# Optimization experiments

Measured on AMD Instinct MI355X. Metric: run time of the kernel, lower is better.

## Reference

```python
import jax, jax.numpy as jnp
import numpy as np

B, S, D = 4, 256, 768      # batch, seq, activation_dim
F = 8192                   # dict_size (both modules)
K = 64                     # topk
C = 128                    # connections per downstream feature


def _topk_keep(post, k):
    """Keep top-k entries per row, zero elsewhere. post: [N, F]."""
    vals, idx = jax.lax.top_k(post, k)
    n = post.shape[0]
    return jnp.zeros_like(post).at[jnp.arange(n)[:, None], idx].set(vals)


def setup_inputs() -> dict:
    key = jax.random.key(0)
    ks = jax.random.split(key, 10)
    s = 1.0 / np.sqrt(D)
    return {
        "initial_acts": jax.random.normal(ks[0], (B, S, D), jnp.float32),
        "x_up": jax.random.normal(ks[1], (B, S, D), jnp.float32),
        "ln_scale": jax.random.uniform(ks[2], (B, S), jnp.float32, 0.5, 1.5),
        "W_enc_up": jax.random.normal(ks[3], (F, D), jnp.float32) * s,
        "b_enc_up": jnp.zeros((F,), jnp.float32),
        "W_dec_up": jax.random.normal(ks[4], (D, F), jnp.float32) * s,
        "b_dec_up": jax.random.normal(ks[5], (D,), jnp.float32) * 0.01,
        "W_enc_down": jax.random.normal(ks[6], (F, D), jnp.float32) * s,
        "b_enc_down": jnp.zeros((F,), jnp.float32),
        "W_dec_down": jax.random.normal(ks[7], (D, F), jnp.float32) * s,
        "b_dec_down": jax.random.normal(ks[8], (D,), jnp.float32) * 0.01,
        "conn": jax.random.randint(ks[9], (F, C), 0, F),  # all valid (no -1 pad)
    }


def reference(initial_acts, x_up, ln_scale,
              W_enc_up, b_enc_up, W_dec_up, b_dec_up,
              W_enc_down, b_enc_down, W_dec_down, b_dec_down,
              conn):
    b, s, d = initial_acts.shape
    n = b * s
    x0 = initial_acts.reshape(n, d)
    xu = x_up.reshape(n, d)
    ln = ln_scale.reshape(n)

    # --- vanilla_forward on upstream: TopK SAE encode + decode ---
    post_up = jax.nn.relu((xu - b_dec_up) @ W_enc_up.T + b_enc_up)  # [n, F]
    feat_up = _topk_keep(post_up, K)
    recon_up = feat_up @ W_dec_up.T + b_dec_up                      # [n, d]

    # --- pruned downstream path ---
    fd = W_enc_down.shape[0]
    fu = W_dec_up.shape[1]
    # virtual weights: down_encoder @ up_decoder  -> [F_down, F_up]
    virtual = W_enc_down @ W_dec_up
    # connection mask from index tensor [F_down, C]
    mask = jnp.zeros((fd, fu), bool).at[jnp.arange(fd)[:, None], conn].set(True)
    masked = jnp.where(mask, virtual, jnp.zeros((), virtual.dtype))

    approx = x0 @ W_enc_down.T                                      # initial contributions [n, F_down]
    approx = approx + feat_up @ masked.T + W_enc_down @ b_dec_up    # pruned contributions + b_dec term
    approx = approx / ln[:, None] + b_enc_down - W_enc_down @ b_dec_down

    feat_down = _topk_keep(approx, K)
    recon_down = feat_down @ W_dec_down.T + b_dec_down              # [n, d]

    return jnp.stack([recon_up.reshape(b, s, d), recon_down.reshape(b, s, d)])
```

## Files before the change

kernel.cpp:

```cpp
#include <hip/hip_runtime.h>


#define NTOK 1024
#define DIM  768
#define FF   8192
#define KK   64
#define CC   128
#define KSEL_UP 80
#define KSEL_DN 80
#define CAP  128

typedef unsigned short u16;
typedef unsigned int   u32;
typedef __attribute__((ext_vector_type(8))) short short8;
typedef __attribute__((ext_vector_type(4))) float floatx4;

__device__ __forceinline__ float bits2f(u32 v) {
    float f; __builtin_memcpy(&f, &v, 4); return f;
}
__device__ __forceinline__ u32 f2bits(float f) {
    u32 u; __builtin_memcpy(&u, &f, 4); return u;
}
__device__ __forceinline__ float bf2f(u16 u) { return bits2f(((u32)u) << 16); }
__device__ __forceinline__ u16 f2bf(float f) {
    u32 u = f2bits(f);
    u32 lsb = (u >> 16) & 1u;
    u += 0x7fffu + lsb;
    return (u16)(u >> 16);
}
__device__ __forceinline__ u16 f2h(float f) {
    _Float16 h = (_Float16)f;
    u16 u; __builtin_memcpy(&u, &h, 2); return u;
}
__device__ __forceinline__ float h2f(u16 u) {
    _Float16 h; __builtin_memcpy(&h, &u, 2); return (float)h;
}
__device__ __forceinline__ u16 hkey(u16 b) {
    return (b & 0x8000u) ? (u16)~b : (u16)(b | 0x8000u);
}
__device__ __forceinline__ u16 hunkey(u16 k) {
    return (k & 0x8000u) ? (u16)(k ^ 0x8000u) : (u16)~k;
}
__device__ __forceinline__ double dot4d(float4 x, float4 w) {
    return (double)x.x * w.x + (double)x.y * w.y
         + (double)x.z * w.z + (double)x.w * w.w;
}

__global__ __launch_bounds__(256) void convert_kernel(const float* __restrict__ src,
                                                      u16* __restrict__ dst, int n4) {
    int i = blockIdx.x * 256 + threadIdx.x;
    if (i < n4) {
        float4 v = ((const float4*)src)[i];
        ushort4 o;
        o.x = f2bf(v.x); o.y = f2bf(v.y); o.z = f2bf(v.z); o.w = f2bf(v.w);
        ((ushort4*)dst)[i] = o;
    }
}

__global__ __launch_bounds__(256) void transpose_kernel(const float* __restrict__ in,
                                                        float* __restrict__ out) {
    __shared__ float tile[32][33];
    int f0 = blockIdx.x * 32, d0 = blockIdx.y * 32;
    int tx = threadIdx.x, ty = threadIdx.y;
#pragma unroll
    for (int i = 0; i < 4; ++i)
        tile[ty + 8 * i][tx] = in[(size_t)(d0 + ty + 8 * i) * FF + f0 + tx];
    __syncthreads();
#pragma unroll
    for (int i = 0; i < 4; ++i)
        out[(size_t)(f0 + ty + 8 * i) * DIM + d0 + tx] = tile[tx][ty + 8 * i];
}

__global__ __launch_bounds__(256) void transpose16_kernel(const float* __restrict__ in,
                                                          u16* __restrict__ out) {
    __shared__ float tile[32][33];
    int f0 = blockIdx.x * 32, d0 = blockIdx.y * 32;
    int tx = threadIdx.x, ty = threadIdx.y;
#pragma unroll
    for (int i = 0; i < 4; ++i)
        tile[ty + 8 * i][tx] = in[(size_t)(d0 + ty + 8 * i) * FF + f0 + tx];
    __syncthreads();
#pragma unroll
    for (int i = 0; i < 4; ++i)
        out[(size_t)(f0 + ty + 8 * i) * DIM + d0 + tx] = f2bf(tile[tx][ty + 8 * i]);
}

__global__ __launch_bounds__(64) void bias_kernel(const float* __restrict__ Weu,
                                                  const float* __restrict__ Wed,
                                                  const float* __restrict__ bdu,
                                                  const float* __restrict__ bdd,
                                                  const float* __restrict__ bed,
                                                  float* __restrict__ sF,
                                                  float* __restrict__ tuF,
                                                  float* __restrict__ c2F,
                                                  double* __restrict__ s64,
                                                  double* __restrict__ tu64,
                                                  double* __restrict__ td64) {
    int f = blockIdx.x, lane = threadIdx.x;
    double su = 0.0, tu = 0.0, td = 0.0;
    for (int i = lane; i < DIM; i += 64) {
        double bu = (double)bdu[i], bd = (double)bdd[i];
        su += (double)Weu[(size_t)f * DIM + i] * bu;
        double w = (double)Wed[(size_t)f * DIM + i];
        tu += w * bu;
        td += w * bd;
    }
#pragma unroll
    for (int off = 32; off; off >>= 1) {
        su += __shfl_xor(su, off);
        tu += __shfl_xor(tu, off);
        td += __shfl_xor(td, off);
    }
    if (lane == 0) {
        sF[f] = (float)su; tuF[f] = (float)tu;
        c2F[f] = (float)((double)bed[f] - td);
        s64[f] = su; tu64[f] = tu; td64[f] = td;
    }
}

template <int MODE>
__global__ __launch_bounds__(256) void gemm16(const u16* __restrict__ A16,
                                              const u16* __restrict__ Bg16,
                                              u16* __restrict__ Sout,
                                              const float* __restrict__ sF,
                                              const float* __restrict__ b_enc) {
    __shared__ __align__(16) u16 As[128 * 40];
    __shared__ __align__(16) u16 Bs[128 * 40];
    int tid = threadIdx.x;
    int wave = tid >> 6, lane = tid & 63;
    int lm = lane & 15, quad = lane >> 4;
    int m0 = blockIdx.y * 128, n0 = blockIdx.x * 128;
    int wm = (wave >> 1) * 64, wn = (wave & 1) * 64;
    floatx4 acc[4][4];
#pragma unroll
    for (int i = 0; i < 4; ++i)
#pragma unroll
        for (int j = 0; j < 4; ++j)
            acc[i][j] = (floatx4){0.f, 0.f, 0.f, 0.f};
    int r = tid >> 2;
    int s = (tid & 3) * 8;
    const u16* gA = A16 + (size_t)(m0 + r) * DIM + s;
    const u16* gB = Bg16 + (size_t)(n0 + r) * DIM + s;
    for (int k0 = 0; k0 < DIM; k0 += 32) {
        short8 a0 = *(const short8*)(gA + k0);
        short8 a1 = *(const short8*)(gA + (size_t)64 * DIM + k0);
        short8 b0 = *(const short8*)(gB + k0);
        short8 b1 = *(const short8*)(gB + (size_t)64 * DIM + k0);
        __syncthreads();
        *(short8*)&As[r * 40 + s]        = a0;
        *(short8*)&As[(r + 64) * 40 + s] = a1;
        *(short8*)&Bs[r * 40 + s]        = b0;
        *(short8*)&Bs[(r + 64) * 40 + s] = b1;
        __syncthreads();
        short8 af[4], bfr[4];
#pragma unroll
        for (int mi = 0; mi < 4; ++mi)
            af[mi] = *(const short8*)&As[(wm + mi * 16 + lm) * 40 + quad * 8];
#pragma unroll
        for (int ni = 0; ni < 4; ++ni)
            bfr[ni] = *(const short8*)&Bs[(wn + ni * 16 + lm) * 40 + quad * 8];
#pragma unroll
        for (int mi = 0; mi < 4; ++mi)
#pragma unroll
            for (int ni = 0; ni < 4; ++ni)
                acc[mi][ni] = __builtin_amdgcn_mfma_f32_16x16x32_bf16(
                    af[mi], bfr[ni], acc[mi][ni], 0, 0, 0);
    }
#pragma unroll
    for (int ni = 0; ni < 4; ++ni) {
        int col = n0 + wn + ni * 16 + lm;
        float sub = 0.f, bb = 0.f;
        if (MODE == 0) { sub = sF[col]; bb = b_enc[col]; }
#pragma unroll
        for (int mi = 0; mi < 4; ++mi) {
#pragma unroll
            for (int reg = 0; reg < 4; ++reg) {
                int row = m0 + wm + mi * 16 + quad * 4 + reg;
                float v = acc[mi][ni][reg];
                if (MODE == 0) { v = v - sub + bb; v = v > 0.f ? v : 0.f; }
                Sout[(size_t)row * FF + col] = f2h(v);
            }
        }
    }
}

__device__ void find_threshold(u32* hist, int k, u32* sc) {
    int tid = threadIdx.x;
    for (int st = 1; st < 256; st <<= 1) {
        u32 v = 0;
        if (tid < 256) {
            v = hist[tid];
            if (tid + st < 256) v += hist[tid + st];
        }
        __syncthreads();
        if (tid < 256) hist[tid] = v;
        __syncthreads();
    }
    if (tid < 256) {
        u32 ge = hist[tid];
        u32 gn = (tid < 255) ? hist[tid + 1] : 0u;
        if ((int)ge >= k && (int)gn < k) { sc[0] = (u32)tid; sc[1] = (u32)(k - (int)gn); }
    }
    __syncthreads();
}

template <typename KT>
__device__ void radix_collect(const KT* __restrict__ keys, u32* hist, int* eqidx,
                              u32* sc, int ksel, u16* cr, u16* cv,
                              int* cnt_out, int row) {
    int tid = threadIdx.x, bs = blockDim.x;
    if (tid < 256) hist[tid] = 0;
    __syncthreads();
    for (int i = tid; i < FF; i += bs) atomicAdd(&hist[((u32)keys[i] & 0xffffu) >> 8], 1u);
    __syncthreads();
    find_threshold(hist, ksel, sc);
    int hb = (int)sc[0], k1 = (int)sc[1];
    if (tid < 256) hist[tid] = 0;
    __syncthreads();
    for (int i = tid; i < FF; i += bs) {
        u32 k = (u32)keys[i] & 0xffffu;
        if ((int)(k >> 8) == hb) atomicAdd(&hist[k & 255u], 1u);
    }
    __syncthreads();
    find_threshold(hist, k1, sc);
    u32 T = ((u32)hb << 8) | sc[0];
    if (tid == 0) { sc[2] = 0; sc[3] = 0; }
    __syncthreads();
    for (int i = tid; i < FF; i += bs) {
        u32 k = (u32)keys[i] & 0xffffu;
        if (k > T) {
            u32 p = atomicAdd(&sc[2], 1u);
            if (p < CAP) { cr[p] = (u16)i; cv[p] = hunkey((u16)k); }
        } else if (k == T) {
            u32 p = atomicAdd(&sc[3], 1u);
            if (p < 256) eqidx[p] = i;
        }
    }
    __syncthreads();
    if (tid == 0) {
        int G = (int)sc[2]; if (G > CAP) G = CAP;
        int ne = (int)sc[3]; if (ne > 256) ne = 256;
        int total = G;
        for (int q = 0; q < ne && total < CAP; ++q) {
            int i = eqidx[q];
            cr[total] = (u16)i;
            cv[total] = hunkey((u16)((u32)keys[i] & 0xffffu));
            ++total;
        }
        cnt_out[row] = total;
    }
}

__device__ __forceinline__ bool sort_before(double av, int ai, double bv, int bi) {
    return (av > bv) || (av == bv && ai < bi);
}
__device__ void bitonic128(double* sv, int* si, int tid) {
    for (int k = 2; k <= 128; k <<= 1) {
        for (int j = k >> 1; j > 0; j >>= 1) {
            __syncthreads();
            if (tid < 64) {
                int i = ((tid & ~(j - 1)) << 1) | (tid & (j - 1));
                int l = i, rr = i + j;
                bool bfirst = sort_before(sv[rr], si[rr], sv[l], si[l]);
                bool doswap = ((i & k) == 0) ? bfirst : !bfirst;
                if (doswap) {
                    double tv = sv[l]; sv[l] = sv[rr]; sv[rr] = tv;
                    int ti = si[l]; si[l] = si[rr]; si[rr] = ti;
                }
            }
        }
    }
    __syncthreads();
}

__global__ __launch_bounds__(512) void select_up2(const u16* __restrict__ S16,
                                                  const float* __restrict__ xu,
                                                  const float* __restrict__ Weu,
                                                  const double* __restrict__ s64,
                                                  const float* __restrict__ beu,
                                                  float* __restrict__ vals,
                                                  int* __restrict__ idxs) {
    __shared__ u16 keys[FF];
    __shared__ u32 hist[256];
    __shared__ int eqidx[256];
    __shared__ u32 sc[4];
    __shared__ u16 cr[CAP];
    __shared__ u16 cv[CAP];
    __shared__ double sv[128];
    __shared__ int si[128];
    __shared__ int cntS;
    int t = blockIdx.x, tid = threadIdx.x, wave = tid >> 6, lane = tid & 63;
    const ushort4* src = (const ushort4*)(S16 + (size_t)t * FF);
    for (int i = tid; i < FF / 4; i += 512) {
        ushort4 u = src[i];
        keys[i * 4]     = hkey(u.x);
        keys[i * 4 + 1] = hkey(u.y);
        keys[i * 4 + 2] = hkey(u.z);
        keys[i * 4 + 3] = hkey(u.w);
    }
    __syncthreads();
    radix_collect<u16>(keys, hist, eqidx, sc, KSEL_UP, cr, cv, &cntS, 0);
    __syncthreads();
    int nc = cntS; if (nc > 128) nc = 128;
    for (int c = tid; c < 128; c += 512) {
        if (c < nc) { si[c] = (int)cr[c]; }
        else { sv[c] = -1.0e300; si[c] = 0x7fffffff; }
    }
    __syncthreads();
    const float4* xr4 = (const float4*)(xu + (size_t)t * DIM);
    float4 x0 = xr4[lane], x1 = xr4[lane + 64], x2 = xr4[lane + 128];
    for (int c = wave; c < nc; c += 8) {
        int f = si[c];
        const float4* wr4 = (const float4*)(Weu + (size_t)f * DIM);
        float4 w0 = wr4[lane], w1 = wr4[lane + 64], w2 = wr4[lane + 128];
        double p = dot4d(x0, w0) + dot4d(x1, w1) + dot4d(x2, w2);
#pragma unroll
        for (int off = 32; off; off >>= 1) p += __shfl_xor(p, off);
        if (lane == 0) {
            double v = p - s64[f] + (double)beu[f];
            v = v > 0.0 ? v : 0.0;
            sv[c] = v;
        }
    }
    __syncthreads();
    bitonic128(sv, si, tid);
    if (tid < KK) {
        vals[(size_t)t * KK + tid] = (float)sv[tid];
        idxs[(size_t)t * KK + tid] = si[tid];
    }
}

__global__ __launch_bounds__(128) void dedup_deg_kernel(const int* __restrict__ conn,
                                                        u32* __restrict__ deg) {
    __shared__ int row[CC];
    int fd = blockIdx.x, c = threadIdx.x;
    int v = conn[(size_t)fd * CC + c];
    row[c] = v;
    __syncthreads();
    bool dup = false;
    for (int j = 0; j < c; ++j) dup |= (row[j] == v);
    if (!dup) atomicAdd(&deg[v], 1u);
}

__global__ __launch_bounds__(256) void scan_kernel(const u32* __restrict__ deg,
                                                   u32* __restrict__ offs) {
    __shared__ u32 sdeg[FF];
    __shared__ u32 part[256];
    int tid = threadIdx.x;
    for (int i = tid; i < FF; i += 256) sdeg[i] = deg[i];
    __syncthreads();
    u32 s = 0;
    for (int j = 0; j < 32; ++j) s += sdeg[tid * 32 + j];
    part[tid] = s;
    __syncthreads();
    if (tid == 0) {
        u32 run = 0;
        for (int i = 0; i < 256; ++i) { u32 v = part[i]; part[i] = run; run += v; }
        offs[FF] = run;
    }
    __syncthreads();
    u32 run = part[tid];
    for (int j = 0; j < 32; ++j) { offs[tid * 32 + j] = run; run += sdeg[tid * 32 + j]; }
}

__global__ __launch_bounds__(128) void fill_kernel(const int* __restrict__ conn,
                                                   const u32* __restrict__ offs,
                                                   u32* __restrict__ cursor,
                                                   u16* __restrict__ inv_fd,
                                                   u16* __restrict__ cclean) {
    __shared__ int row[CC];
    int fd = blockIdx.x, c = threadIdx.x;
    int v = conn[(size_t)fd * CC + c];
    row[c] = v;
    __syncthreads();
    bool dup = false;
    for (int j = 0; j < c; ++j) dup |= (row[j] == v);
    cclean[(size_t)fd * CC + c] = dup ? (u16)0xFFFF : (u16)v;
    if (!dup) {
        u32 slot = atomicAdd(&cursor[v], 1u);
        inv_fd[offs[v] + slot] = (u16)fd;
    }
}

__global__ __launch_bounds__(256) void vconn_chunk(const u16* __restrict__ Wed16,
                                                   const float* __restrict__ WduT,
                                                   const u32* __restrict__ offs,
                                                   const u16* __restrict__ inv_fd,
                                                   u32* __restrict__ pe,
                                                   int chunk, int first) {
    __shared__ float row[192];
    int fu = blockIdx.x, tid = threadIdx.x;
    if (tid < 192) row[tid] = WduT[(size_t)fu * DIM + chunk * 192 + tid];
    __syncthreads();
    u32 s = offs[fu], e = offs[fu + 1];
    int wave = tid >> 6, lane = tid & 63;
    int sub = lane >> 4, sl = lane & 15;
    for (u32 p0 = s + (u32)wave * 4; p0 < e; p0 += 16) {
        u32 p = p0 + (u32)sub;
        bool valid = p < e;
        float a = 0.f;
        int fd = 0;
        u32 old = 0;
        if (valid) {
            if (first) fd = (int)inv_fd[p];
            else { old = pe[p]; fd = (int)(old >> 16); }
            const u16* wr = Wed16 + (size_t)fd * DIM + chunk * 192;
#pragma unroll
            for (int i = 0; i < 12; ++i)
                a = fmaf(bf2f(wr[sl + 16 * i]), row[sl + 16 * i], a);
        }
        a += __shfl_xor(a, 1);
        a += __shfl_xor(a, 2);
        a += __shfl_xor(a, 4);
        a += __shfl_xor(a, 8);
        if (valid && sl == 0) {
            float v = first ? a : (bf2f((u16)(old & 0xffffu)) + a);
            pe[p] = ((u32)fd << 16) | (u32)f2bf(v);
        }
    }
}

__global__ __launch_bounds__(512) void phase2sel2(const u16* __restrict__ S16,
                                                  const float* __restrict__ vals_up,
                                                  const int* __restrict__ idx_up,
                                                  const u32* __restrict__ offs,
                                                  const u32* __restrict__ pe,
                                                  const float* __restrict__ tuF,
                                                  const float* __restrict__ c2F,
                                                  const float* __restrict__ ln,
                                                  u16* __restrict__ cand,
                                                  u16* __restrict__ candv,
                                                  int* __restrict__ cnt) {
    __shared__ u32 accbits[FF];
    __shared__ float zl[KK];
    __shared__ u32 offs_s[KK];
    __shared__ u32 ends_s[KK];
    __shared__ u32 hist[256];
    __shared__ int eqidx[256];
    __shared__ u32 sc[4];
    float* facc = (float*)accbits;
    int t = blockIdx.x, tid = threadIdx.x, wave = tid >> 6, lane = tid & 63;
    for (int i = tid; i < FF; i += 512) accbits[i] = 0u;
    if (tid < KK) {
        int f = idx_up[(size_t)t * KK + tid];
        zl[tid] = vals_up[(size_t)t * KK + tid];
        offs_s[tid] = offs[f];
        ends_s[tid] = offs[f + 1];
    }
    __syncthreads();
    for (int j = wave; j < KK; j += 8) {
        u32 s = offs_s[j], e = ends_s[j];
        float zj = zl[j];
        u32 p = s + (u32)lane;
        u32 v0 = 0, v1 = 0, v2 = 0;
        bool h0 = p < e, h1 = p + 64 < e, h2 = p + 128 < e;
        if (h0) v0 = pe[p];
        if (h1) v1 = pe[p + 64];
        if (h2) v2 = pe[p + 128];
        if (h0) atomicAdd(&facc[v0 >> 16], zj * bf2f((u16)(v0 & 0xffffu)));
        if (h1) atomicAdd(&facc[v1 >> 16], zj * bf2f((u16)(v1 & 0xffffu)));
        if (h2) atomicAdd(&facc[v2 >> 16], zj * bf2f((u16)(v2 & 0xffffu)));
        for (u32 q = p + 192; q < e; q += 64) {
            u32 v = pe[q];
            atomicAdd(&facc[v >> 16], zj * bf2f((u16)(v & 0xffffu)));
        }
    }
    __syncthreads();
    float lnv = ln[t];
    const ushort4* bs4 = (const ushort4*)(S16 + (size_t)t * FF);
    const float4* tu4 = (const float4*)tuF;
    const float4* c24 = (const float4*)c2F;
    for (int i = tid; i < FF / 4; i += 512) {
        ushort4 bas = bs4[i];
        float4 tu = tu4[i], c2 = c24[i];
        int i4 = i * 4;
        float a0 = facc[i4], a1 = facc[i4 + 1], a2 = facc[i4 + 2], a3 = facc[i4 + 3];
        accbits[i4]     = (u32)hkey(f2h((h2f(bas.x) + a0 + tu.x) / lnv + c2.x));
        accbits[i4 + 1] = (u32)hkey(f2h((h2f(bas.y) + a1 + tu.y) / lnv + c2.y));
        accbits[i4 + 2] = (u32)hkey(f2h((h2f(bas.z) + a2 + tu.z) / lnv + c2.z));
        accbits[i4 + 3] = (u32)hkey(f2h((h2f(bas.w) + a3 + tu.w) / lnv + c2.w));
    }
    __syncthreads();
    radix_collect<u32>(accbits, hist, eqidx, sc, KSEL_DN,
                       cand + (size_t)t * CAP, candv + (size_t)t * CAP, cnt, t);
}

__global__ __launch_bounds__(512) void fixup_dn2(const float* __restrict__ x0g,
                                                 const float* __restrict__ Wed,
                                                 const float* __restrict__ WduT,
                                                 const double* __restrict__ tu64,
                                                 const double* __restrict__ td64,
                                                 const float* __restrict__ bed,
                                                 const float* __restrict__ ln,
                                                 const u16* __restrict__ cclean,
                                                 const float* __restrict__ vals_up,
                                                 const int* __restrict__ idx_up,
                                                 const u16* __restrict__ cand,
                                                 const u16* __restrict__ candv,
                                                 const int* __restrict__ cnt,
                                                 float* __restrict__ vals,
                                                 int* __restrict__ idxs) {
    __shared__ u32 bm[256];
    __shared__ int fl[KK];
    __shared__ float zl[KK];
    __shared__ double sv[128];
    __shared__ int si[128];
    __shared__ int mlo, mhi;
    int t = blockIdx.x, tid = threadIdx.x, wave = tid >> 6, lane = tid & 63;
    if (tid < 256) bm[tid] = 0;
    if (tid == 0) { mlo = 128; mhi = -1; }
    __syncthreads();
    if (tid < KK) {
        int f = idx_up[(size_t)t * KK + tid];
        fl[tid] = f; zl[tid] = vals_up[(size_t)t * KK + tid];
        atomicOr(&bm[f >> 5], 1u << (f & 31));
    }
    int nc = cnt[t]; if (nc > 128) nc = 128;
    for (int c = tid; c < 128; c += 512) {
        if (c < nc) {
            sv[c] = (double)h2f(candv[(size_t)t * CAP + c]);
            si[c] = (int)cand[(size_t)t * CAP + c];
        } else { sv[c] = -1.0e300; si[c] = 0x7fffffff; }
    }
    __syncthreads();
    int myfl = fl[lane];
    double lnt = (double)ln[t];
    double Mdn = 0.08 / lnt + 0.016;
    bitonic128(sv, si, tid);
    double b = sv[63];
    if (tid < 128 && tid < nc) {
        double d = sv[tid] - b; if (d < 0) d = -d;
        if (d <= Mdn) { atomicMin(&mlo, tid); atomicMax(&mhi, tid); }
    }
    __syncthreads();
    int blo = mlo, bhi = mhi;
    const float4* xr4 = (const float4*)(x0g + (size_t)t * DIM);
    float4 x0 = xr4[lane], x1 = xr4[lane + 64], x2 = xr4[lane + 128];
    for (int c = blo + wave; c <= bhi; c += 8) {
        int f = si[c];
        const u16* crow = cclean + (size_t)f * CC;
        int e0 = (int)crow[lane], e1 = (int)crow[lane + 64];
        const float4* wr4 = (const float4*)(Wed + (size_t)f * DIM);
        float4 w0 = wr4[lane], w1 = wr4[lane + 64], w2 = wr4[lane + 128];
        double p = dot4d(x0, w0) + dot4d(x1, w1) + dot4d(x2, w2);
        bool h0 = (e0 != 0xFFFF) && ((bm[e0 >> 5] >> (e0 & 31)) & 1u);
        bool h1 = (e1 != 0xFFFF) && ((bm[e1 >> 5] >> (e1 & 31)) & 1u);
        unsigned long long m0 = __ballot(h0), m1 = __ballot(h1);
        while (m0 | m1) {
            int fu;
            if (m0) {
                int bb = __ffsll((long long)m0) - 1; m0 &= m0 - 1;
                fu = __shfl(e0, bb);
            } else {
                int bb = __ffsll((long long)m1) - 1; m1 &= m1 - 1;
                fu = __shfl(e1, bb);
            }
            unsigned long long zm = __ballot(myfl == fu);
            if (!zm) continue;
            float z = zl[__ffsll((long long)zm) - 1];
            const float4* du4 = (const float4*)(WduT + (size_t)fu * DIM);
            float4 d0 = du4[lane], d1 = du4[lane + 64], d2 = du4[lane + 128];
            double vp = dot4d(w0, d0) + dot4d(w1, d1) + dot4d(w2, d2);
            p += (double)z * vp;
        }
#pragma unroll
        for (int off = 32; off; off >>= 1) p += __shfl_xor(p, off);
        if (lane == 0)
            sv[c] = (p + tu64[f]) / lnt + (double)bed[f] - td64[f];
    }
    __syncthreads();
    bitonic128(sv, si, tid);
    if (tid < KK) {
        vals[(size_t)t * KK + tid] = (float)sv[tid];
        idxs[(size_t)t * KK + tid] = si[tid];
    }
}

__global__ __launch_bounds__(256) void decode_both(const float* __restrict__ vals_up,
                                                   const int* __restrict__ idx_up,
                                                   const float* __restrict__ vals_dn,
                                                   const int* __restrict__ idx_dn,
                                                   const u16* __restrict__ WduT16,
                                                   const u16* __restrict__ WddT16,
                                                   const float* __restrict__ bdu,
                                                   const float* __restrict__ bdd,
                                                   float* __restrict__ outp) {
    __shared__ float z[KK];
    __shared__ int fidx[KK];
    int b = blockIdx.x, tid = threadIdx.x;
    int which = b >> 10, t = b & 1023;
    const float* vals = which ? vals_dn : vals_up;
    const int* idxs = which ? idx_dn : idx_up;
    const u16* WdT = which ? WddT16 : WduT16;
    const float* bd = which ? bdd : bdu;
    float* o = outp + (size_t)which * NTOK * DIM + (size_t)t * DIM;
    if (tid < KK) { z[tid] = vals[(size_t)t * KK + tid]; fidx[tid] = idxs[(size_t)t * KK + tid]; }
    __syncthreads();
    float a0 = 0.f, a1 = 0.f, a2 = 0.f;
    for (int j = 0; j < KK; ++j) {
        const u16* wr = WdT + (size_t)fidx[j] * DIM;
        float zj = z[j];
        a0 = fmaf(zj, bf2f(wr[tid]), a0);
        a1 = fmaf(zj, bf2f(wr[tid + 256]), a1);
        a2 = fmaf(zj, bf2f(wr[tid + 512]), a2);
    }
    o[tid]       = a0 + bd[tid];
    o[tid + 256] = a1 + bd[tid + 256];
    o[tid + 512] = a2 + bd[tid + 512];
}

extern "C" void kernel_launch(void* const* d_in, const int* in_sizes, int n_in,
                              void* d_out, int out_size, void* d_ws, size_t ws_size,
                              hipStream_t stream) {
    const float* x0  = (const float*)d_in[0];
    const float* xu  = (const float*)d_in[1];
    const float* ln  = (const float*)d_in[2];
    const float* Weu = (const float*)d_in[3];
    const float* beu = (const float*)d_in[4];
    const float* Wdu = (const float*)d_in[5];
    const float* bdu = (const float*)d_in[6];
    const float* Wed = (const float*)d_in[7];
    const float* bed = (const float*)d_in[8];
    const float* Wdd = (const float*)d_in[9];
    const float* bdd = (const float*)d_in[10];
    const int* conn = (const int*)d_in[11];
    float* out = (float*)d_out;

    char* w = (char*)d_ws;
    size_t off = 0;
    auto take = [&](size_t bytes) { char* p = w + off; off = (off + bytes + 255) & ~(size_t)255; return p; };
    u16*   S16     = (u16*)take((size_t)NTOK * FF * 2);
    u16*   B16     = (u16*)take((size_t)FF * DIM * 2);
    u16*   WddT16  = S16;
    u16*   WduT16  = B16;
    float* WduT    = (float*)take((size_t)FF * DIM * 4);
    u16*   Weu16   = (u16*)WduT;
    u16*   inv_fd  = (u16*)take((size_t)FF * CC * 2);
    u16*   cclean  = (u16*)take((size_t)FF * CC * 2);
    u32*   pe      = (u32*)take((size_t)FF * CC * 4);
    u16*   Xu16    = (u16*)pe;
    u16*   X016    = Xu16 + (size_t)NTOK * DIM;
    u16*   cand_d  = (u16*)take((size_t)NTOK * CAP * 2);
    u16*   candv_d = (u16*)take((size_t)NTOK * CAP * 2);
    int*   cnt_d   = (int*)take(NTOK * 4);
    float* vals_up = (float*)take((size_t)NTOK * KK * 4);
    int*   idx_up  = (int*)take((size_t)NTOK * KK * 4);
    float* vals_dn = (float*)take((size_t)NTOK * KK * 4);
    int*   idx_dn  = (int*)take((size_t)NTOK * KK * 4);
    float* sF      = (float*)take(FF * 4);
    float* tuF     = (float*)take(FF * 4);
    float* c2F     = (float*)take(FF * 4);
    double* s64    = (double*)take(FF * 8);
    double* tu64   = (double*)take(FF * 8);
    double* td64   = (double*)take(FF * 8);
    u32*   deg     = (u32*)take(FF * 4);
    u32*   cursor  = (u32*)take(FF * 4);
    u32*   offs    = (u32*)take((FF + 8) * 4);

    dim3 tgrid(FF / 32, DIM / 32), tblk(32, 8);
    dim3 ggrid(FF / 128, NTOK / 128);
    int nB4 = FF * DIM / 4;
    int nX4 = NTOK * DIM / 4;

    bias_kernel<<<FF, 64, 0, stream>>>(Weu, Wed, bdu, bdd, bed, sF, tuF, c2F,
                                       s64, tu64, td64);
    hipMemsetAsync(deg, 0, 2 * FF * sizeof(u32), stream);
    dedup_deg_kernel<<<FF, CC, 0, stream>>>(conn, deg);
    scan_kernel<<<1, 256, 0, stream>>>(deg, offs);
    fill_kernel<<<FF, CC, 0, stream>>>(conn, offs, cursor, inv_fd, cclean);

    convert_kernel<<<(nB4 + 255) / 256, 256, 0, stream>>>(Weu, Weu16, nB4);
    convert_kernel<<<(nX4 + 255) / 256, 256, 0, stream>>>(xu, Xu16, nX4);
    gemm16<0><<<ggrid, 256, 0, stream>>>(Xu16, Weu16, S16, sF, beu);
    transpose_kernel<<<tgrid, tblk, 0, stream>>>(Wdu, WduT);
    select_up2<<<NTOK, 512, 0, stream>>>(S16, xu, Weu, s64, beu, vals_up, idx_up);

    convert_kernel<<<(nB4 + 255) / 256, 256, 0, stream>>>(Wed, B16, nB4);
    convert_kernel<<<(nX4 + 255) / 256, 256, 0, stream>>>(x0, X016, nX4);
    gemm16<1><<<ggrid, 256, 0, stream>>>(X016, B16, S16, sF, beu);
    vconn_chunk<<<FF, 256, 0, stream>>>(B16, WduT, offs, inv_fd, pe, 0, 1);
    vconn_chunk<<<FF, 256, 0, stream>>>(B16, WduT, offs, inv_fd, pe, 1, 0);
    vconn_chunk<<<FF, 256, 0, stream>>>(B16, WduT, offs, inv_fd, pe, 2, 0);
    vconn_chunk<<<FF, 256, 0, stream>>>(B16, WduT, offs, inv_fd, pe, 3, 0);
    convert_kernel<<<(nB4 + 255) / 256, 256, 0, stream>>>(WduT, WduT16, nB4);
    phase2sel2<<<NTOK, 512, 0, stream>>>(S16, vals_up, idx_up, offs, pe,
                                         tuF, c2F, ln, cand_d, candv_d, cnt_d);
    fixup_dn2<<<NTOK, 512, 0, stream>>>(x0, Wed, WduT, tu64, td64, bed, ln, cclean,
                                        vals_up, idx_up, cand_d, candv_d, cnt_d,
                                        vals_dn, idx_dn);

    transpose16_kernel<<<tgrid, tblk, 0, stream>>>(Wdd, WddT16);
    decode_both<<<2 * NTOK, 256, 0, stream>>>(vals_up, idx_up, vals_dn, idx_dn,
                                              WduT16, WddT16, bdu, bdd, out);
}
```

Baseline: 710.0 us.

## Merge paired bf16 conversions, parallelize scan prefix, tighten downstream fixup margin

Merges each pair of fp32-to-bf16 conversion launches into a single kernel covering both buffers, removing two kernel launches. Replaces the serial single-thread prefix over 256 partial sums with a parallel Hillis-Steele scan in shared memory. Also narrows the downstream boundary margin Mdn, which shrinks the range of candidates near the top-k threshold that get recomputed exactly. The narrower margin reduces fixup work but raises the risk of wrong top-k selection near ties.

```diff
diff --git a/kernel.cpp b/kernel.cpp
--- a/kernel.cpp
+++ b/kernel.cpp
@@ -55,6 +55,20 @@
         o.x = f2bf(v.x); o.y = f2bf(v.y); o.z = f2bf(v.z); o.w = f2bf(v.w);
         ((ushort4*)dst)[i] = o;
     }
+}
+
+__global__ __launch_bounds__(256) void convert2_kernel(const float* __restrict__ s1,
+                                                       u16* __restrict__ d1, int n1,
+                                                       const float* __restrict__ s2,
+                                                       u16* __restrict__ d2, int n2) {
+    int i = blockIdx.x * 256 + threadIdx.x;
+    const float* src; u16* dst; int j;
+    if (i < n1) { src = s1; dst = d1; j = i; }
+    else { j = i - n1; if (j >= n2) return; src = s2; dst = d2; }
+    float4 v = ((const float4*)src)[j];
+    ushort4 o;
+    o.x = f2bf(v.x); o.y = f2bf(v.y); o.z = f2bf(v.z); o.w = f2bf(v.w);
+    ((ushort4*)dst)[j] = o;
 }
 
 __global__ __launch_bounds__(256) void transpose_kernel(const float* __restrict__ in,
@@ -353,13 +367,15 @@
     for (int j = 0; j < 32; ++j) s += sdeg[tid * 32 + j];
     part[tid] = s;
     __syncthreads();
-    if (tid == 0) {
-        u32 run = 0;
-        for (int i = 0; i < 256; ++i) { u32 v = part[i]; part[i] = run; run += v; }
-        offs[FF] = run;
-    }
-    __syncthreads();
-    u32 run = part[tid];
+    for (int st = 1; st < 256; st <<= 1) {
+        u32 v = 0;
+        if (tid >= st) v = part[tid - st];
+        __syncthreads();
+        part[tid] += v;
+        __syncthreads();
+    }
+    if (tid == 255) offs[FF] = part[255];
+    u32 run = part[tid] - s;
     for (int j = 0; j < 32; ++j) { offs[tid * 32 + j] = run; run += sdeg[tid * 32 + j]; }
 }
 
@@ -525,7 +541,7 @@
     __syncthreads();
     int myfl = fl[lane];
     double lnt = (double)ln[t];
-    double Mdn = 0.08 / lnt + 0.016;
+    double Mdn = 0.07 / lnt + 0.014;
     bitonic128(sv, si, tid);
     double b = sv[63];
     if (tid < 128 && tid < nc) {
@@ -661,6 +677,7 @@
     dim3 ggrid(FF / 128, NTOK / 128);
     int nB4 = FF * DIM / 4;
     int nX4 = NTOK * DIM / 4;
+    int nBoth = nB4 + nX4;
 
     bias_kernel<<<FF, 64, 0, stream>>>(Weu, Wed, bdu, bdd, bed, sF, tuF, c2F,
                                        s64, tu64, td64);
@@ -669,14 +686,14 @@
     scan_kernel<<<1, 256, 0, stream>>>(deg, offs);
     fill_kernel<<<FF, CC, 0, stream>>>(conn, offs, cursor, inv_fd, cclean);
 
-    convert_kernel<<<(nB4 + 255) / 256, 256, 0, stream>>>(Weu, Weu16, nB4);
-    convert_kernel<<<(nX4 + 255) / 256, 256, 0, stream>>>(xu, Xu16, nX4);
+    convert2_kernel<<<(nBoth + 255) / 256, 256, 0, stream>>>(Weu, Weu16, nB4,
+                                                             xu, Xu16, nX4);
     gemm16<0><<<ggrid, 256, 0, stream>>>(Xu16, Weu16, S16, sF, beu);
     transpose_kernel<<<tgrid, tblk, 0, stream>>>(Wdu, WduT);
     select_up2<<<NTOK, 512, 0, stream>>>(S16, xu, Weu, s64, beu, vals_up, idx_up);
 
-    convert_kernel<<<(nB4 + 255) / 256, 256, 0, stream>>>(Wed, B16, nB4);
-    convert_kernel<<<(nX4 + 255) / 256, 256, 0, stream>>>(x0, X016, nX4);
+    convert2_kernel<<<(nBoth + 255) / 256, 256, 0, stream>>>(Wed, B16, nB4,
+                                                             x0, X016, nX4);
     gemm16<1><<<ggrid, 256, 0, stream>>>(X016, B16, S16, sF, beu);
     vconn_chunk<<<FF, 256, 0, stream>>>(B16, WduT, offs, inv_fd, pe, 0, 1);
     vconn_chunk<<<FF, 256, 0, stream>>>(B16, WduT, offs, inv_fd, pe, 1, 0);
```

After: 704.5 us. Within noise of the previous version (-0.8%).
